# Kernel tuning notes

Measured on AMD Instinct MI355X. Metric: run time of the kernel, lower is better.

The kernel has to match this reference:

```python
import jax, jax.numpy as jnp
import numpy as np

N = 100_000          # nodes
E = 1_600_000        # edges (avg degree 16)
NODE_SCA, NODE_VEC = 4, 3
EDGE_SCA, EDGE_VEC = 6, 3
OUT_SCA, OUT_VEC = 16, 16
CUTOFF = 10.0
EPS = 1e-6
SLOPE_VN = 0.2       # VNLeakyReLU negative slope (SurfGen default)
SLOPE_SCA = 0.01     # nn.LeakyReLU default


def setup_inputs() -> dict:
    key = jax.random.key(0)
    ks = jax.random.split(key, 22)
    rn = lambda k, s: jax.random.normal(k, s, dtype=jnp.float32)
    return {
        # forward args
        'node_sca': rn(ks[0], (N, NODE_SCA)),
        'node_vec': rn(ks[1], (N, NODE_VEC, 3)),
        'edge_sca': rn(ks[2], (E, EDGE_SCA)),
        'edge_vec': rn(ks[3], (E, EDGE_VEC, 3)),
        'gds_dist': jax.random.uniform(ks[4], (E,), dtype=jnp.float32) * 12.0,
        'edge_index': jax.random.randint(ks[5], (2, E), 0, N),
        # message projections (Linear weights stored [in,out])
        'W_nss': rn(ks[6], (NODE_SCA, OUT_SCA)) * 0.3, 'b_nss': rn(ks[7], (OUT_SCA,)) * 0.1,
        'W_ess': rn(ks[8], (EDGE_SCA, OUT_SCA)) * 0.3, 'b_ess': rn(ks[9], (OUT_SCA,)) * 0.1,
        'W_nsv': rn(ks[10], (NODE_SCA, OUT_SCA)) * 0.3, 'b_nsv': rn(ks[11], (OUT_SCA,)) * 0.1,
        'W_esv': rn(ks[12], (EDGE_SCA, OUT_SCA)) * 0.3, 'b_esv': rn(ks[13], (OUT_SCA,)) * 0.1,
        'W_nvv': rn(ks[14], (NODE_VEC, OUT_VEC)) * 0.3,   # VNLinear (no bias)
        'W_evv': rn(ks[15], (EDGE_VEC, OUT_VEC)) * 0.3,
        # GVPerceptronVN(16,16,16,16): GVLinear (dim_hid = 16) + VN LeakyReLU
        'W_lv':  rn(ks[16], (OUT_VEC, OUT_VEC)) * 0.25,   # lin_vector   (no bias)
        'W_lv2': rn(ks[17], (OUT_VEC, OUT_VEC)) * 0.25,   # lin_vector2  (no bias)
        'W_ls':  rn(ks[18], (OUT_VEC + OUT_SCA, OUT_SCA)) * 0.25,  # lin_scalar (no bias)
        'W_gate': rn(ks[19], (OUT_SCA, OUT_VEC)) * 0.25, 'b_gate': rn(ks[20], (OUT_VEC,)) * 0.1,
        'W_dir': rn(ks[21], (OUT_VEC, OUT_VEC)) * 0.25,   # VNLeakyReLU direction (no bias)
    }


def vn_linear(x, W):
    # x: [n, c_in, 3], W: [c_in, c_out] -> [n, c_out, 3]
    return jnp.einsum('nci,co->noi', x, W)


def reference(node_sca, node_vec, edge_sca, edge_vec, gds_dist, edge_index,
              W_nss, b_nss, W_ess, b_ess, W_nsv, b_nsv, W_esv, b_esv,
              W_nvv, W_evv, W_lv, W_lv2, W_ls, W_gate, b_gate, W_dir):
    src = edge_index[0]
    num_nodes = node_sca.shape[0]

    # cosine cutoff coefficient
    coeff = 0.5 * (jnp.cos(gds_dist * (jnp.pi / CUTOFF)) + 1.0)
    coeff = coeff * (gds_dist <= CUTOFF) * (gds_dist >= 0.0)  # [E]

    # scalar message: gather node proj, mix with edge proj, cutoff-weight
    node_ss = node_sca @ W_nss + b_nss                          # [N,16]
    edge_ss = edge_sca @ W_ess + b_ess                          # [E,16]
    msg_sca = node_ss[src] * edge_ss * coeff[:, None]           # [E,16]

    # vector message
    node_vv = vn_linear(node_vec, W_nvv)                        # [N,16,3]
    edge_vv = vn_linear(edge_vec, W_evv)                        # [E,16,3]
    node_sv = node_sca @ W_nsv + b_nsv                          # [N,16]
    edge_sv = edge_sca @ W_esv + b_esv                          # [E,16]
    msg_vec = (node_vv[src] * edge_sv[:, :, None]
               + node_sv[src][:, :, None] * edge_vv) * coeff[:, None, None]  # [E,16,3]

    # scatter_sum into source nodes (matches original's edge_index[0])
    aggr_sca = jax.ops.segment_sum(msg_sca, src, num_segments=num_nodes)  # [N,16]
    aggr_vec = jax.ops.segment_sum(msg_vec, src, num_segments=num_nodes)  # [N,16,3]

    # --- GVPerceptronVN: GVLinear ---
    v_inter = vn_linear(aggr_vec, W_lv)                          # [N,16,3]
    v_norm = jnp.sqrt(jnp.sum(v_inter * v_inter, axis=-1))       # [N,16]
    out_sca = jnp.concatenate([v_norm, aggr_sca], axis=-1) @ W_ls  # [N,16]
    out_vec = vn_linear(v_inter, W_lv2)                          # [N,16,3]
    gate = jax.nn.sigmoid(out_sca @ W_gate + b_gate)[:, :, None]
    out_vec = gate * out_vec

    # --- VNLeakyReLU on vectors ---
    d = vn_linear(out_vec, W_dir)                                # [N,16,3]
    dot = jnp.sum(out_vec * d, axis=-1, keepdims=True)
    mask = (dot >= 0).astype(out_vec.dtype)
    d_norm_sq = jnp.sum(d * d, axis=-1, keepdims=True)
    out_vec = SLOPE_VN * out_vec + (1.0 - SLOPE_VN) * (
        mask * out_vec + (1.0 - mask) * (out_vec - (dot / (d_norm_sq + EPS)) * d))

    # LeakyReLU on scalars
    out_sca = jnp.where(out_sca >= 0, out_sca, SLOPE_SCA * out_sca)
    return out_sca, out_vec
```

## Files before the change

### kernel.cpp

```cpp
#include <hip/hip_runtime.h>
#include <math.h>

#define CUTOFF_F 10.0f
#define PI_OVER_CUTOFF 0.31415926535897931f
#define KID 32

__global__ __launch_bounds__(256) void fill_ids(
    const float* __restrict__ gds,
    const int* __restrict__ eidx,
    const float* __restrict__ edge_sca,
    const float* __restrict__ edge_vec,
    int* __restrict__ count,
    int* __restrict__ bucket,
    float* __restrict__ aggr,
    int E)
{
    int e = blockIdx.x * blockDim.x + threadIdx.x;
    if (e >= E) return;

    float d = gds[e];
    if (d > CUTOFF_F || d < 0.0f) return;

    int src = eidx[e];
    int slot = atomicAdd(&count[src], 1);
    if (slot < KID) {
        bucket[(size_t)src * KID + slot] = e;
    } else {
        float c = 0.5f * (__cosf(d * PI_OVER_CUTOFF) + 1.0f);
        const float* es = edge_sca + (size_t)e * 6;
        const float* ev = edge_vec + (size_t)e * 9;
        float* base = aggr + (size_t)src * 16;
#pragma unroll
        for (int i = 0; i < 6; ++i) atomicAdd(base + i, c * es[i]);
        atomicAdd(base + 6, c);
#pragma unroll
        for (int i = 0; i < 9; ++i) atomicAdd(base + 7 + i, c * ev[i]);
    }
}

__global__ __launch_bounds__(256) void edge_aggregate(
    const float* __restrict__ edge_sca, const float* __restrict__ edge_vec,
    const float* __restrict__ gds, const int* __restrict__ eidx,
    float* __restrict__ aggr, int E)
{
    int e = blockIdx.x * blockDim.x + threadIdx.x;
    if (e >= E) return;
    int src = eidx[e];
    float d = gds[e];
    float coeff = 0.0f;
    if (d >= 0.0f && d <= CUTOFF_F)
        coeff = 0.5f * (__cosf(d * PI_OVER_CUTOFF) + 1.0f);
    float* base = aggr + (size_t)src * 16;
    const float* es = edge_sca + (size_t)e * 6;
    const float* ev = edge_vec + (size_t)e * 9;
#pragma unroll
    for (int c = 0; c < 6; ++c) atomicAdd(base + c, coeff * es[c]);
    atomicAdd(base + 6, coeff);
#pragma unroll
    for (int k = 0; k < 9; ++k) atomicAdd(base + 7 + k, coeff * ev[k]);
}

__global__ __launch_bounds__(256) void node_fused(
    const float* __restrict__ node_sca,
    const float* __restrict__ node_vec,
    const float* __restrict__ edge_sca,
    const float* __restrict__ edge_vec,
    const float* __restrict__ gds,
    const int* __restrict__ count,
    const int* __restrict__ bucket,
    const float* __restrict__ aggr,
    const float* __restrict__ W_nss, const float* __restrict__ b_nss,
    const float* __restrict__ W_ess, const float* __restrict__ b_ess,
    const float* __restrict__ W_nsv, const float* __restrict__ b_nsv,
    const float* __restrict__ W_esv, const float* __restrict__ b_esv,
    const float* __restrict__ W_nvv, const float* __restrict__ W_evv,
    const float* __restrict__ W_lv,  const float* __restrict__ W_lv2,
    const float* __restrict__ W_ls,
    const float* __restrict__ W_gate, const float* __restrict__ b_gate,
    const float* __restrict__ W_dir,
    float* __restrict__ out,
    int N, int mode)
{
    __shared__ float sW_nss[64],  sb_nss[16];
    __shared__ float sW_ess[96],  sb_ess[16];
    __shared__ float sW_nsv[64],  sb_nsv[16];
    __shared__ float sW_esv[96],  sb_esv[16];
    __shared__ float sW_nvv[48],  sW_evv[48];
    __shared__ float sW_lv[256],  sW_lv2[256];
    __shared__ float sW_ls[512];
    __shared__ float sW_gate[256], sb_gate[16];
    __shared__ float sW_dir[256];

    __shared__ float s_in  [16 * 33];
    __shared__ float s_avec[16 * 49];
    __shared__ float s_cat [16 * 33];
    __shared__ float s_vint[16 * 49];
    __shared__ float s_osca[16 * 17];
    __shared__ float s_ovec[16 * 49];

    __shared__ int   s_eid[KID * 17];
    __shared__ float s_ec [KID * 17];

    const int t = threadIdx.x;
    {
        for (int i = t; i < 64;  i += 256) { sW_nss[i] = W_nss[i]; sW_nsv[i] = W_nsv[i]; }
        for (int i = t; i < 96;  i += 256) { sW_ess[i] = W_ess[i]; sW_esv[i] = W_esv[i]; }
        for (int i = t; i < 48;  i += 256) { sW_nvv[i] = W_nvv[i]; sW_evv[i] = W_evv[i]; }
        for (int i = t; i < 256; i += 256) {
            sW_lv[i]   = W_lv[i];
            sW_lv2[i]  = W_lv2[i];
            sW_gate[i] = W_gate[i];
            sW_dir[i]  = W_dir[i];
        }
        for (int i = t; i < 512; i += 256) sW_ls[i] = W_ls[i];
        if (t < 16) {
            sb_nss[t]  = b_nss[t];
            sb_ess[t]  = b_ess[t];
            sb_nsv[t]  = b_nsv[t];
            sb_esv[t]  = b_esv[t];
            sb_gate[t] = b_gate[t];
        }
    }

    const int slot = t >> 4;
    const int o    = t & 15;
    const int n    = blockIdx.x * 16 + slot;
    const bool valid = (n < N);

    if (valid) {
        if (o < 4) s_in[slot * 33 + o]     = node_sca[(size_t)n * 4 + o];
        if (o < 9) s_in[slot * 33 + 4 + o] = node_vec[(size_t)n * 9 + o];
    }

    if (mode == 4) {
        int cnt = 0;
        if (valid) {
            cnt = count[n];
            if (cnt > KID) cnt = KID;
            const int* bk = bucket + (size_t)n * KID;
            for (int s = o; s < cnt; s += 16) {
                int e = bk[s];
                float d = gds[e];
                s_eid[s * 17 + slot] = e;
                s_ec [s * 17 + slot] = 0.5f * (__cosf(d * PI_OVER_CUTOFF) + 1.0f);
            }
        }
        __syncthreads();
        if (valid) {
            float acc = aggr[(size_t)n * 16 + o];
            const float* fsrc = (o < 6) ? edge_sca : edge_vec;
            const int    st   = (o < 6) ? 6 : 9;
            const int    off  = (o < 6) ? o : (o - 7);
            for (int s = 0; s < cnt; ++s) {
                int   e = s_eid[s * 17 + slot];
                float c = s_ec [s * 17 + slot];
                float f = (o == 6) ? 1.0f : fsrc[(size_t)e * st + off];
                acc += c * f;
            }
            s_in[slot * 33 + 13 + o] = acc;
        }
    } else {
        if (valid) s_in[slot * 33 + 13 + o] = aggr[(size_t)n * 16 + o];
    }
    __syncthreads();

    const float* in = s_in + slot * 33;

    float nss = sb_nss[o], nsv = sb_nsv[o];
#pragma unroll
    for (int c = 0; c < 4; ++c) {
        float x = in[c];
        nss += x * sW_nss[c * 16 + o];
        nsv += x * sW_nsv[c * 16 + o];
    }
    float nvv0 = 0.f, nvv1 = 0.f, nvv2 = 0.f;
#pragma unroll
    for (int c = 0; c < 3; ++c) {
        float w = sW_nvv[c * 16 + o];
        nvv0 += in[4 + c * 3 + 0] * w;
        nvv1 += in[4 + c * 3 + 1] * w;
        nvv2 += in[4 + c * 3 + 2] * w;
    }
    float cc = in[19];
    float es = cc * sb_ess[o], ev = cc * sb_esv[o];
#pragma unroll
    for (int c = 0; c < 6; ++c) {
        float a = in[13 + c];
        es += a * sW_ess[c * 16 + o];
        ev += a * sW_esv[c * 16 + o];
    }
    float EV0 = 0.f, EV1 = 0.f, EV2 = 0.f;
#pragma unroll
    for (int c = 0; c < 3; ++c) {
        float w = sW_evv[c * 16 + o];
        EV0 += in[20 + c * 3 + 0] * w;
        EV1 += in[20 + c * 3 + 1] * w;
        EV2 += in[20 + c * 3 + 2] * w;
    }

    float asca = nss * es;
    float av0 = nvv0 * ev + nsv * EV0;
    float av1 = nvv1 * ev + nsv * EV1;
    float av2 = nvv2 * ev + nsv * EV2;
    s_avec[slot * 49 + o * 3 + 0] = av0;
    s_avec[slot * 49 + o * 3 + 1] = av1;
    s_avec[slot * 49 + o * 3 + 2] = av2;
    s_cat[slot * 33 + 16 + o] = asca;
    __syncthreads();

    float vi0 = 0.f, vi1 = 0.f, vi2 = 0.f;
#pragma unroll
    for (int c = 0; c < 16; ++c) {
        float w = sW_lv[c * 16 + o];
        const float* a = &s_avec[slot * 49 + c * 3];
        vi0 += a[0] * w; vi1 += a[1] * w; vi2 += a[2] * w;
    }
    float vnorm = sqrtf(vi0 * vi0 + vi1 * vi1 + vi2 * vi2);
    s_vint[slot * 49 + o * 3 + 0] = vi0;
    s_vint[slot * 49 + o * 3 + 1] = vi1;
    s_vint[slot * 49 + o * 3 + 2] = vi2;
    s_cat[slot * 33 + o] = vnorm;
    __syncthreads();

    float osca = 0.f;
#pragma unroll
    for (int c = 0; c < 32; ++c)
        osca += s_cat[slot * 33 + c] * sW_ls[c * 16 + o];
    float ov0 = 0.f, ov1 = 0.f, ov2 = 0.f;
#pragma unroll
    for (int c = 0; c < 16; ++c) {
        float w = sW_lv2[c * 16 + o];
        const float* a = &s_vint[slot * 49 + c * 3];
        ov0 += a[0] * w; ov1 += a[1] * w; ov2 += a[2] * w;
    }
    s_osca[slot * 17 + o] = osca;
    __syncthreads();

    float g = sb_gate[o];
#pragma unroll
    for (int c = 0; c < 16; ++c)
        g += s_osca[slot * 17 + c] * sW_gate[c * 16 + o];
    g = 1.0f / (1.0f + __expf(-g));
    ov0 *= g; ov1 *= g; ov2 *= g;
    s_ovec[slot * 49 + o * 3 + 0] = ov0;
    s_ovec[slot * 49 + o * 3 + 1] = ov1;
    s_ovec[slot * 49 + o * 3 + 2] = ov2;
    __syncthreads();

    float dv0 = 0.f, dv1 = 0.f, dv2 = 0.f;
#pragma unroll
    for (int c = 0; c < 16; ++c) {
        float w = sW_dir[c * 16 + o];
        const float* a = &s_ovec[slot * 49 + c * 3];
        dv0 += a[0] * w; dv1 += a[1] * w; dv2 += a[2] * w;
    }
    float dot = ov0 * dv0 + ov1 * dv1 + ov2 * dv2;
    if (dot < 0.0f) {
        float dn = dv0 * dv0 + dv1 * dv1 + dv2 * dv2;
        float f = 0.8f * dot / (dn + 1e-6f);
        ov0 -= f * dv0; ov1 -= f * dv1; ov2 -= f * dv2;
    }

    if (valid) {
        float so = (osca >= 0.0f) ? osca : 0.01f * osca;
        out[(size_t)n * 16 + o] = so;
        size_t vb = (size_t)N * 16 + (size_t)n * 48 + (size_t)o * 3;
        out[vb + 0] = ov0;
        out[vb + 1] = ov1;
        out[vb + 2] = ov2;
    }
}

extern "C" void kernel_launch(void* const* d_in, const int* in_sizes, int n_in,
                              void* d_out, int out_size, void* d_ws, size_t ws_size,
                              hipStream_t stream)
{
    const float* node_sca = (const float*)d_in[0];
    const float* node_vec = (const float*)d_in[1];
    const float* edge_sca = (const float*)d_in[2];
    const float* edge_vec = (const float*)d_in[3];
    const float* gds      = (const float*)d_in[4];
    const int*   eidx     = (const int*)d_in[5];

    const int N = in_sizes[0] / 4;
    const int E = in_sizes[4];

    int*   count4  = (int*)d_ws;
    float* aggr4   = (float*)(count4 + N);
    int*   bucket4 = (int*)(aggr4 + (size_t)N * 16);
    size_t need4   = (size_t)N * 4 + (size_t)N * 64 + (size_t)N * KID * 4;

    float* aggr0  = (float*)d_ws;
    size_t need0  = (size_t)N * 64;

    if (ws_size >= need4) {
        hipMemsetAsync(count4, 0, (size_t)N * 4 + (size_t)N * 64, stream);
        fill_ids<<<(E + 255) / 256, 256, 0, stream>>>(
            gds, eidx, edge_sca, edge_vec, count4, bucket4, aggr4, E);
        node_fused<<<(N + 15) / 16, 256, 0, stream>>>(
            node_sca, node_vec, edge_sca, edge_vec, gds,
            count4, bucket4, aggr4,
            (const float*)d_in[6],  (const float*)d_in[7],
            (const float*)d_in[8],  (const float*)d_in[9],
            (const float*)d_in[10], (const float*)d_in[11],
            (const float*)d_in[12], (const float*)d_in[13],
            (const float*)d_in[14], (const float*)d_in[15],
            (const float*)d_in[16], (const float*)d_in[17],
            (const float*)d_in[18],
            (const float*)d_in[19], (const float*)d_in[20],
            (const float*)d_in[21],
            (float*)d_out, N, 4);
        return;
    }

    (void)need0;
    hipMemsetAsync(aggr0, 0, (size_t)N * 64, stream);
    edge_aggregate<<<(E + 255) / 256, 256, 0, stream>>>(
        edge_sca, edge_vec, gds, eidx, aggr0, E);
    node_fused<<<(N + 15) / 16, 256, 0, stream>>>(
        node_sca, node_vec, edge_sca, edge_vec, gds,
        (const int*)d_ws, (const int*)d_ws, aggr0,
        (const float*)d_in[6],  (const float*)d_in[7],
        (const float*)d_in[8],  (const float*)d_in[9],
        (const float*)d_in[10], (const float*)d_in[11],
        (const float*)d_in[12], (const float*)d_in[13],
        (const float*)d_in[14], (const float*)d_in[15],
        (const float*)d_in[16], (const float*)d_in[17],
        (const float*)d_in[18],
        (const float*)d_in[19], (const float*)d_in[20],
        (const float*)d_in[21],
        (float*)d_out, N, 0);
}
```

Baseline: 335.4 us.

## Bucket precomputed fp16 edge payloads per node instead of edge ids

```diff
diff --git a/kernel.cpp b/kernel.cpp
--- a/kernel.cpp
+++ b/kernel.cpp
@@ -1,40 +1,51 @@
 #include <hip/hip_runtime.h>
+#include <hip/hip_fp16.h>
 #include <math.h>
 
 #define CUTOFF_F 10.0f
 #define PI_OVER_CUTOFF 0.31415926535897931f
-#define KID 32
-
-__global__ __launch_bounds__(256) void fill_ids(
+#define KCAP 32
+
+__global__ __launch_bounds__(256) void bucket_scatter(
     const float* __restrict__ gds,
     const int* __restrict__ eidx,
     const float* __restrict__ edge_sca,
     const float* __restrict__ edge_vec,
     int* __restrict__ count,
-    int* __restrict__ bucket,
+    __half* __restrict__ bucket,
     float* __restrict__ aggr,
     int E)
 {
-    int e = blockIdx.x * blockDim.x + threadIdx.x;
+    int e = blockIdx.x * 256 + threadIdx.x;
     if (e >= E) return;
 
     float d = gds[e];
-    if (d > CUTOFF_F || d < 0.0f) return;
-
+    if (d < 0.0f || d > CUTOFF_F) return;
+
+    float c = 0.5f * (__cosf(d * PI_OVER_CUTOFF) + 1.0f);
     int src = eidx[e];
+    const float* es = edge_sca + (size_t)e * 6;
+    const float* ev = edge_vec + (size_t)e * 9;
+
+    float f[16];
+#pragma unroll
+    for (int i = 0; i < 6; ++i) f[i] = c * es[i];
+    f[6] = c;
+#pragma unroll
+    for (int i = 0; i < 9; ++i) f[7 + i] = c * ev[i];
+
     int slot = atomicAdd(&count[src], 1);
-    if (slot < KID) {
-        bucket[(size_t)src * KID + slot] = e;
+    if (slot < KCAP) {
+        union { __half h[16]; uint4 u[2]; } pk;
+#pragma unroll
+        for (int i = 0; i < 16; ++i) pk.h[i] = __float2half(f[i]);
+        uint4* pb = (uint4*)(bucket + ((size_t)src * KCAP + slot) * 16);
+        pb[0] = pk.u[0];
+        pb[1] = pk.u[1];
     } else {
-        float c = 0.5f * (__cosf(d * PI_OVER_CUTOFF) + 1.0f);
-        const float* es = edge_sca + (size_t)e * 6;
-        const float* ev = edge_vec + (size_t)e * 9;
         float* base = aggr + (size_t)src * 16;
 #pragma unroll
-        for (int i = 0; i < 6; ++i) atomicAdd(base + i, c * es[i]);
-        atomicAdd(base + 6, c);
-#pragma unroll
-        for (int i = 0; i < 9; ++i) atomicAdd(base + 7 + i, c * ev[i]);
+        for (int i = 0; i < 16; ++i) atomicAdd(base + i, f[i]);
     }
 }
 
@@ -63,11 +74,8 @@
 __global__ __launch_bounds__(256) void node_fused(
     const float* __restrict__ node_sca,
     const float* __restrict__ node_vec,
-    const float* __restrict__ edge_sca,
-    const float* __restrict__ edge_vec,
-    const float* __restrict__ gds,
     const int* __restrict__ count,
-    const int* __restrict__ bucket,
+    const __half* __restrict__ payload,
     const float* __restrict__ aggr,
     const float* __restrict__ W_nss, const float* __restrict__ b_nss,
     const float* __restrict__ W_ess, const float* __restrict__ b_ess,
@@ -98,9 +106,6 @@
     __shared__ float s_osca[16 * 17];
     __shared__ float s_ovec[16 * 49];
 
-    __shared__ int   s_eid[KID * 17];
-    __shared__ float s_ec [KID * 17];
-
     const int t = threadIdx.x;
     {
         for (int i = t; i < 64;  i += 256) { sW_nss[i] = W_nss[i]; sW_nsv[i] = W_nsv[i]; }
@@ -132,32 +137,40 @@
         if (o < 9) s_in[slot * 33 + 4 + o] = node_vec[(size_t)n * 9 + o];
     }
 
-    if (mode == 4) {
-        int cnt = 0;
+    if (mode == 1) {
+        float acc[8] = {0.f, 0.f, 0.f, 0.f, 0.f, 0.f, 0.f, 0.f};
+        const int h  = o & 1;
+        const int sg = o >> 1;
         if (valid) {
-            cnt = count[n];
-            if (cnt > KID) cnt = KID;
-            const int* bk = bucket + (size_t)n * KID;
-            for (int s = o; s < cnt; s += 16) {
-                int e = bk[s];
-                float d = gds[e];
-                s_eid[s * 17 + slot] = e;
-                s_ec [s * 17 + slot] = 0.5f * (__cosf(d * PI_OVER_CUTOFF) + 1.0f);
+            int cnt = count[n];
+            if (cnt > KCAP) cnt = KCAP;
+            const uint4* pu = (const uint4*)payload + (size_t)n * (KCAP * 2);
+#pragma unroll
+            for (int k = 0; k < 4; ++k) {
+                int s = sg + 8 * k;
+                if (s < cnt) {
+                    uint4 v = pu[o + 16 * k];
+                    const __half2* hp = (const __half2*)&v;
+#pragma unroll
+                    for (int j = 0; j < 4; ++j) {
+                        float2 f2 = __half22float2(hp[j]);
+                        acc[2 * j]     += f2.x;
+                        acc[2 * j + 1] += f2.y;
+                    }
+                }
             }
         }
-        __syncthreads();
-        if (valid) {
-            float acc = aggr[(size_t)n * 16 + o];
-            const float* fsrc = (o < 6) ? edge_sca : edge_vec;
-            const int    st   = (o < 6) ? 6 : 9;
-            const int    off  = (o < 6) ? o : (o - 7);
-            for (int s = 0; s < cnt; ++s) {
-                int   e = s_eid[s * 17 + slot];
-                float c = s_ec [s * 17 + slot];
-                float f = (o == 6) ? 1.0f : fsrc[(size_t)e * st + off];
-                acc += c * f;
-            }
-            s_in[slot * 33 + 13 + o] = acc;
+#pragma unroll
+        for (int m = 2; m <= 8; m <<= 1) {
+#pragma unroll
+            for (int j = 0; j < 8; ++j)
+                acc[j] += __shfl_xor(acc[j], m, 16);
+        }
+        if (valid && o < 2) {
+#pragma unroll
+            for (int j = 0; j < 8; ++j)
+                s_in[slot * 33 + 13 + 8 * h + j] =
+                    acc[j] + aggr[(size_t)n * 16 + 8 * h + j];
         }
     } else {
         if (valid) s_in[slot * 33 + 13 + o] = aggr[(size_t)n * 16 + o];
@@ -285,21 +298,18 @@
     const int N = in_sizes[0] / 4;
     const int E = in_sizes[4];
 
-    int*   count4  = (int*)d_ws;
-    float* aggr4   = (float*)(count4 + N);
-    int*   bucket4 = (int*)(aggr4 + (size_t)N * 16);
-    size_t need4   = (size_t)N * 4 + (size_t)N * 64 + (size_t)N * KID * 4;
-
-    float* aggr0  = (float*)d_ws;
-    size_t need0  = (size_t)N * 64;
-
-    if (ws_size >= need4) {
-        hipMemsetAsync(count4, 0, (size_t)N * 4 + (size_t)N * 64, stream);
-        fill_ids<<<(E + 255) / 256, 256, 0, stream>>>(
-            gds, eidx, edge_sca, edge_vec, count4, bucket4, aggr4, E);
+    int*    count  = (int*)d_ws;
+    float*  aggr   = (float*)(count + N);
+    __half* bucket = (__half*)(aggr + (size_t)N * 16);
+    size_t  hdr    = (size_t)N * 4 + (size_t)N * 64;
+    size_t  need   = hdr + (size_t)N * KCAP * 16 * sizeof(__half);
+
+    if (ws_size >= need) {
+        hipMemsetAsync(count, 0, hdr, stream);
+        bucket_scatter<<<(E + 255) / 256, 256, 0, stream>>>(
+            gds, eidx, edge_sca, edge_vec, count, bucket, aggr, E);
         node_fused<<<(N + 15) / 16, 256, 0, stream>>>(
-            node_sca, node_vec, edge_sca, edge_vec, gds,
-            count4, bucket4, aggr4,
+            node_sca, node_vec, count, bucket, aggr,
             (const float*)d_in[6],  (const float*)d_in[7],
             (const float*)d_in[8],  (const float*)d_in[9],
             (const float*)d_in[10], (const float*)d_in[11],
@@ -309,17 +319,17 @@
             (const float*)d_in[18],
             (const float*)d_in[19], (const float*)d_in[20],
             (const float*)d_in[21],
-            (float*)d_out, N, 4);
+            (float*)d_out, N, 1);
         return;
     }
 
-    (void)need0;
-    hipMemsetAsync(aggr0, 0, (size_t)N * 64, stream);
+    size_t zb = hdr;
+    if (zb > ws_size) zb = ws_size;
+    hipMemsetAsync(count, 0, zb, stream);
     edge_aggregate<<<(E + 255) / 256, 256, 0, stream>>>(
-        edge_sca, edge_vec, gds, eidx, aggr0, E);
+        edge_sca, edge_vec, gds, eidx, aggr, E);
     node_fused<<<(N + 15) / 16, 256, 0, stream>>>(
-        node_sca, node_vec, edge_sca, edge_vec, gds,
-        (const int*)d_ws, (const int*)d_ws, aggr0,
+        node_sca, node_vec, count, bucket, aggr,
         (const float*)d_in[6],  (const float*)d_in[7],
         (const float*)d_in[8],  (const float*)d_in[9],
         (const float*)d_in[10], (const float*)d_in[11],
```

Result: faster. 289.1 us (-13.8%).
